# Kernel optimization log

Hardware: AMD Instinct MI355X
Metric: run time of the kernel (lower is better)

The kernel has to match this reference:

```python
import jax, jax.numpy as jnp
import numpy as np

N, E = 20000, 320000
C, IN_NF, HID_NF, OUT_NF, CH_NF, RAD_NF = 14, 128, 128, 128, 16, 128
CONSTANT = 1.0
LN_EPS = 1e-5
SCALE = 0.02


def _pool_matrix(c, dtype):
    # RollerPooling buffer: pool_matrix[i] averages a sliding window of size c-i
    ones = np.ones((c, c), dtype=np.float32)
    mats = [(np.triu(ones) - np.triu(ones, k=c - i)) / float(c - i) for i in range(c)]
    return jnp.asarray(np.stack(mats), dtype=dtype)


def setup_inputs() -> dict:
    key = jax.random.key(0)
    ks = jax.random.split(key, 32)
    h = jax.random.normal(ks[0], (N, IN_NF), jnp.float32)
    x = jax.random.normal(ks[1], (N, C, 3), jnp.float32)
    row = jax.random.randint(ks[2], (E,), 0, N)
    off = jax.random.randint(ks[3], (E,), 1, N)
    col = (row + off) % N  # guarantees row != col (avoids zero-distance edges)
    channel_attr = jax.random.normal(ks[4], (N, C, CH_NF), jnp.float32)
    w = jax.random.uniform(ks[5], (N, C), jnp.float32, 0.1, 1.0)
    keep = jax.random.uniform(ks[6], (N, C)) > 0.3
    keep = keep.at[:, 0].set(True)  # every node has >=1 active channel
    channel_weights = w * keep.astype(jnp.float32)

    def lin(k, o, i):
        k1, k2 = jax.random.split(k)
        return (jax.random.normal(k1, (o, i), jnp.float32) * SCALE,
                jax.random.normal(k2, (o,), jnp.float32) * SCALE)

    radial_W, radial_b = lin(ks[7], RAD_NF, CH_NF * CH_NF)
    e1_W, e1_b = lin(ks[8], HID_NF, 2 * IN_NF + RAD_NF)
    e2_W, e2_b = lin(ks[9], HID_NF, HID_NF)
    att_W, att_b = lin(ks[10], 1, HID_NF)
    c1_W, c1_b = lin(ks[11], HID_NF, HID_NF)
    c2_W, c2_b = lin(ks[12], C, HID_NF)
    n1_W, n1_b = lin(ks[13], HID_NF, IN_NF + HID_NF)
    n2_W, n2_b = lin(ks[14], OUT_NF, HID_NF)
    ln_g = jnp.ones((OUT_NF,), jnp.float32)
    ln_b = jnp.zeros((OUT_NF,), jnp.float32)
    return dict(h=h, x=x, row=row, col=col, channel_attr=channel_attr,
                channel_weights=channel_weights,
                radial_W=radial_W, radial_b=radial_b,
                e1_W=e1_W, e1_b=e1_b, e2_W=e2_W, e2_b=e2_b,
                att_W=att_W, att_b=att_b,
                c1_W=c1_W, c1_b=c1_b, c2_W=c2_W, c2_b=c2_b,
                n1_W=n1_W, n1_b=n1_b, n2_W=n2_W, n2_b=n2_b,
                ln_g=ln_g, ln_b=ln_b)


def _scatter_mean(v, idx, n):
    s = jnp.zeros((n,) + v.shape[1:], v.dtype).at[idx].add(v)
    cnt = jnp.zeros((n,), v.dtype).at[idx].add(1.0)
    cnt = jnp.maximum(cnt, 1.0)
    return s / cnt.reshape((n,) + (1,) * (v.ndim - 1))


def _forward(h, x, row, col, channel_attr, channel_weights,
             radial_W, radial_b, e1_W, e1_b, e2_W, e2_b, att_W, att_b,
             c1_W, c1_b, c2_W, c2_b, n1_W, n1_b, n2_W, n2_b, ln_g, ln_b):
    n, c, d = x.shape
    silu = jax.nn.silu
    coord_r = x[row]           # [E, C, 3]
    coord_c = x[col]
    # pairwise channel distances [E, C, C]
    dist = jnp.linalg.norm(coord_r[:, :, None, :] - coord_c[:, None, :, :], axis=-1)
    cw_r = channel_weights[row]
    cw_c = channel_weights[col]
    coord_msg = dist * (cw_r[:, :, None] * cw_c[:, None, :])
    # attr_r^T @ coord_msg @ attr_c -> [E, CH_NF, CH_NF]
    radial = jnp.einsum('eca,ecd,edb->eab', channel_attr[row], coord_msg, channel_attr[col])
    radial = radial.reshape(radial.shape[0], -1)
    rnorm = jnp.linalg.norm(radial, axis=-1, keepdims=True) + CONSTANT
    radial = (radial @ radial_W.T + radial_b) / rnorm  # [E, RAD_NF]
    # pooled column coord over active channels
    mask = (channel_weights != 0).astype(x.dtype)      # [N, C]
    csum = mask.sum(-1)                                # [N]
    pooled_col = (coord_c * mask[col][:, :, None]).sum(1) / csum[col][:, None]  # [E, 3]
    coord_diff = coord_r - pooled_col[:, None, :]      # [E, C, 3]
    # edge MLP (dropout = identity in eval)
    ef = jnp.concatenate([h[row], h[col], radial], axis=-1)
    ef = silu(ef @ e1_W.T + e1_b)
    ef = silu(ef @ e2_W.T + e2_b)
    ef = ef * jax.nn.sigmoid(ef @ att_W.T + att_b)     # att_mlp (hidden_nf == input_nf)
    # coord MLP + roller pooling
    ch = silu(ef @ c1_W.T + c1_b) @ c2_W.T + c2_b      # [E, C]
    tsize = csum[row].astype(jnp.int32) - 1            # [E] in [0, C-1]
    pool_mat = _pool_matrix(c, x.dtype)                # [C, C, C]
    pooled = jnp.einsum('eij,ej->ei', pool_mat[tsize], ch)  # [E, C]
    trans = coord_diff * pooled[:, :, None]            # [E, C, 3]
    x_out = x + _scatter_mean(trans, row, n)
    agg = _scatter_mean(ef, col, n)
    nh = jnp.concatenate([h, agg], axis=-1)
    nh = silu(nh @ n1_W.T + n1_b) @ n2_W.T + n2_b
    y = h + nh
    mu = y.mean(-1, keepdims=True)
    var = ((y - mu) ** 2).mean(-1, keepdims=True)
    h_out = (y - mu) / jnp.sqrt(var + LN_EPS) * ln_g + ln_b
    return h_out, x_out


def reference(h, x, row, col, channel_attr, channel_weights,
              radial_W, radial_b, e1_W, e1_b, e2_W, e2_b, att_W, att_b,
              c1_W, c1_b, c2_W, c2_b, n1_W, n1_b, n2_W, n2_b, ln_g, ln_b):
    return _forward(h, x, row, col, channel_attr, channel_weights,
                    radial_W, radial_b, e1_W, e1_b, e2_W, e2_b, att_W, att_b,
                    c1_W, c1_b, c2_W, c2_b, n1_W, n1_b, n2_W, n2_b, ln_g, ln_b)
```

## Files before the change

### kernel.cpp

```cpp
#include <hip/hip_runtime.h>
#include <math.h>

#define NN 20000
#define NE 320000

typedef const float* fp;
typedef short short8 __attribute__((ext_vector_type(8)));
typedef short short4v __attribute__((ext_vector_type(4)));
typedef float f32x4 __attribute__((ext_vector_type(4)));

__device__ __forceinline__ short F2B(float f) {
    unsigned u = __float_as_uint(f);
    return (short)((u + 0x7fffu + ((u >> 16) & 1u)) >> 16);
}
__device__ __forceinline__ short F2Bf(float f) {
    return (short)((__float_as_uint(f) + 0x8000u) >> 16);
}
__device__ __forceinline__ float B2F(short s) {
    return __uint_as_float(((unsigned)(unsigned short)s) << 16);
}
__device__ __forceinline__ float siluf(float v) { return v / (1.f + __expf(-v)); }

#if defined(__has_builtin)
#if __has_builtin(__builtin_amdgcn_mfma_f32_16x16x16bf16_1k)
#define MFMA16_BUILTIN 1
__device__ __forceinline__ f32x4 mfma16(short4v a, short4v b, f32x4 c) {
    return __builtin_amdgcn_mfma_f32_16x16x16bf16_1k(a, b, c, 0, 0, 0);
}
#elif __has_builtin(__builtin_amdgcn_mfma_f32_16x16x16_bf16)
#define MFMA16_BUILTIN 1
__device__ __forceinline__ f32x4 mfma16(short4v a, short4v b, f32x4 c) {
    return __builtin_amdgcn_mfma_f32_16x16x16_bf16(a, b, c, 0, 0, 0);
}
#endif
#endif
#ifndef MFMA16_BUILTIN
__device__ __forceinline__ f32x4 mfma16(short4v a, short4v b, f32x4 c) {
    f32x4 d;
    asm volatile("s_nop 1\n\tv_mfma_f32_16x16x16_bf16 %0, %1, %2, %3\n\ts_nop 7\n\ts_nop 7"
                 : "=v"(d) : "v"(a), "v"(b), "v"(c));
    return d;
}
#endif

__global__ void k_prep_w(fp e1W, fp e2W, fp c1W, fp c2W, fp n1W, fp n2W,
                         short* __restrict__ wb) {
    int i = blockIdx.x * 256 + threadIdx.x;
    if (i >= 149504) return;
    if (i >= 32768 && i < 65536) return;
    float v;
    if (i < 32768)       { int o = i >> 8, k = i & 255; v = e1W[o * 384 + k]; }
    else if (i < 81920)  v = e2W[i - 65536];
    else if (i < 98304)  v = c1W[i - 81920];
    else if (i < 100352) { int q = i - 98304; v = (q < 1792) ? c2W[q] : 0.f; }
    else if (i < 133120) v = n1W[i - 100352];
    else                 v = n2W[i - 133120];
    wb[i] = F2B(v);
}

__global__ void k_fold(fp e1W, fp rW, fp rB, short* __restrict__ wb,
                       float* __restrict__ bc) {
    int o = blockIdx.x, k = threadIdx.x;
    float acc = 0.f;
    for (int m = 0; m < 128; m++) acc += e1W[o * 384 + 256 + m] * rW[m * 256 + k];
    wb[32768 + o * 256 + k] = F2B(acc);
    if (k == 0) {
        float b = 0.f;
        for (int m = 0; m < 128; m++) b += e1W[o * 384 + 256 + m] * rB[m];
        bc[o] = b;
    }
}

__global__ void k_prep_h(fp h, short* __restrict__ hb) {
    int i = blockIdx.x * 256 + threadIdx.x;
    if (i < NN * 128) hb[i] = F2B(h[i]);
}

__global__ void k_prep_attrT(fp attr, fp cw, short* __restrict__ aT) {
    int i = blockIdx.x * 256 + threadIdx.x;
    if (i >= NN * 256) return;
    int n = i >> 8, rem = i & 255, c = rem >> 4, a = rem & 15;
    float v = (c < 14) ? attr[(size_t)n * 224 + c * 16 + a] * cw[n * 14 + c] : 0.f;
    aT[(size_t)n * 256 + a * 16 + c] = F2B(v);
}

__global__ void k_node_pre(fp x, fp cw, float* __restrict__ csum, float* __restrict__ pool) {
    int n = blockIdx.x * blockDim.x + threadIdx.x;
    if (n >= NN) return;
    float cnt = 0.f, px = 0.f, py = 0.f, pz = 0.f;
#pragma unroll
    for (int c = 0; c < 14; c++) {
        float w = cw[n * 14 + c];
        if (w != 0.f) {
            cnt += 1.f;
            px += x[(n * 14 + c) * 3 + 0];
            py += x[(n * 14 + c) * 3 + 1];
            pz += x[(n * 14 + c) * 3 + 2];
        }
    }
    if (cnt < 1.f) cnt = 1.f;
    csum[n] = cnt;
    pool[n * 3 + 0] = px / cnt;
    pool[n * 3 + 1] = py / cnt;
    pool[n * 3 + 2] = pz / cnt;
}

__global__ void k_count(const int* __restrict__ row, const int* __restrict__ col,
                        int* __restrict__ cnt_r, int* __restrict__ cnt_c) {
    int e = blockIdx.x * 256 + threadIdx.x;
    if (e >= NE) return;
    atomicAdd(&cnt_c[col[e]], 1);
    atomicAdd(&cnt_r[row[e]], 1);
}

__global__ void k_scan(int* __restrict__ cnt0, int* __restrict__ cnt1,
                       int* __restrict__ off0, int* __restrict__ off1) {
    __shared__ int part[256];
    const int tid = threadIdx.x;
    for (int a = 0; a < 2; a++) {
        int* cnt = a ? cnt1 : cnt0;
        int* off = a ? off1 : off0;
        int c0 = tid * 79, c1 = c0 + 79;
        if (c1 > 20000) c1 = 20000;
        int s = 0;
        for (int i = c0; i < c1; i++) s += cnt[i];
        part[tid] = s;
        __syncthreads();
        if (tid == 0) {
            int r = 0;
            for (int i = 0; i < 256; i++) { int t = part[i]; part[i] = r; r += t; }
        }
        __syncthreads();
        int run = part[tid];
        for (int i = c0; i < c1; i++) {
            int cv = cnt[i];
            off[i] = run;
            cnt[i] = run;
            run += cv;
        }
        if (tid == 255) off[20000] = run;
        __syncthreads();
    }
}

__global__ void k_fill(const int* __restrict__ row, const int* __restrict__ col,
                       int* __restrict__ head_r, int* __restrict__ head_c,
                       int* __restrict__ eidx_r,
                       int* __restrict__ row_s, int* __restrict__ col_s) {
    int e = blockIdx.x * 256 + threadIdx.x;
    if (e >= NE) return;
    int r = row[e], c = col[e];
    int pc = atomicAdd(&head_c[c], 1);
    row_s[pc] = r;
    col_s[pc] = c;
    int pr = atomicAdd(&head_r[r], 1);
    eidx_r[pr] = pc;
}

__device__ __forceinline__ void gemm_lds(const short* __restrict__ A, int sA,
                                         const short* __restrict__ W, int Ws, int K,
                                         int mt, int nt0, int nts, f32x4* acc) {
    const int lane = threadIdx.x & 63;
    const short* ap = A + (mt * 16 + (lane & 15)) * sA + ((lane >> 4) * 8);
    for (int k0 = 0; k0 < K; k0 += 32) {
        short8 a = *(const short8*)(ap + k0);
#pragma unroll
        for (int t = 0; t < nts; t++) {
            short8 b = *(const short8*)(W + ((nt0 + t) * 16 + (lane & 15)) * Ws + k0 + ((lane >> 4) * 8));
            acc[t] = __builtin_amdgcn_mfma_f32_16x16x32_bf16(a, b, acc[t], 0, 0, 0);
        }
    }
}
__device__ __forceinline__ void gemm_grow(const short* __restrict__ arow,
                                          const short* __restrict__ W, int Ws, int K,
                                          int nt0, int nts, f32x4* acc) {
    const int lane = threadIdx.x & 63;
    for (int k0 = 0; k0 < K; k0 += 32) {
        short8 a = *(const short8*)(arow + k0);
#pragma unroll
        for (int t = 0; t < nts; t++) {
            short8 b = *(const short8*)(W + ((nt0 + t) * 16 + (lane & 15)) * Ws + k0 + ((lane >> 4) * 8));
            acc[t] = __builtin_amdgcn_mfma_f32_16x16x32_bf16(a, b, acc[t], 0, 0, 0);
        }
    }
}

__global__ __launch_bounds__(256, 2) void k_hw(const short* __restrict__ hb,
                                               const short* __restrict__ wb,
                                               short* __restrict__ H12) {
    __shared__ __attribute__((aligned(16))) short A[32 * 136];
    const int tid = threadIdx.x, lane = tid & 63, w = tid >> 6;
    const int bb = lane & 15, quad = lane >> 4;
    const int mt = w & 1, nh = w >> 1, nb0 = blockIdx.x * 32;
    for (int p = tid; p < 512; p += 256) {
        int i = p >> 4, v = p & 15;
        *(short8*)(A + i * 136 + v * 8) = *(const short8*)(hb + (size_t)(nb0 + i) * 128 + v * 8);
    }
    __syncthreads();
    f32x4 acc[4];
#pragma unroll
    for (int t = 0; t < 4; t++) acc[t] = (f32x4){0.f, 0.f, 0.f, 0.f};
    gemm_lds(A, 136, wb, 256, 128, mt, nh * 4, 4, acc);
#pragma unroll
    for (int t = 0; t < 4; t++)
#pragma unroll
        for (int i = 0; i < 4; i++) {
            int m = mt * 16 + quad * 4 + i, n = (nh * 4 + t) * 16 + bb;
            H12[(size_t)(nb0 + m) * 256 + n] = F2Bf(acc[t][i]);
        }
#pragma unroll
    for (int t = 0; t < 4; t++) acc[t] = (f32x4){0.f, 0.f, 0.f, 0.f};
    gemm_lds(A, 136, wb + 128, 256, 128, mt, nh * 4, 4, acc);
#pragma unroll
    for (int t = 0; t < 4; t++)
#pragma unroll
        for (int i = 0; i < 4; i++) {
            int m = mt * 16 + quad * 4 + i, n = (nh * 4 + t) * 16 + bb;
            H12[(size_t)(nb0 + m) * 256 + 128 + n] = F2Bf(acc[t][i]);
        }
}

__global__ __launch_bounds__(256, 6) void k_radial(
    fp x, const int* __restrict__ row_s, const int* __restrict__ col_s,
    const short* __restrict__ attrT,
    const short* __restrict__ wb, const float* __restrict__ bc,
    short* __restrict__ e1p) {
    __shared__ __attribute__((aligned(16))) short Ar[32 * 264];
    __shared__ float xc2[4][2][48];
    __shared__ float s_inv[32];
    const int tid = threadIdx.x, lane = tid & 63, w = tid >> 6;
    const int bb = lane & 15, quad = lane >> 4;
    const int e0 = blockIdx.x * 32;
    const short* Wc = wb + 32768;

#pragma unroll 2
    for (int m = 0; m < 8; m++) {
        const int ep = e0 + w * 8 + m;
        const int r = row_s[ep], c = col_s[ep];
        const int bufi = m & 1;
        short4v arv = *(const short4v*)(attrT + (size_t)r * 256 + bb * 16 + quad * 4);
        short4v acv = *(const short4v*)(attrT + (size_t)c * 256 + bb * 16 + quad * 4);
        if (lane < 42) xc2[w][bufi][lane] = x[(size_t)c * 42 + lane];
        const int iic = bb < 14 ? bb : 13;
        float xr0 = x[(size_t)r * 42 + iic * 3];
        float xr1 = x[(size_t)r * 42 + iic * 3 + 1];
        float xr2 = x[(size_t)r * 42 + iic * 3 + 2];
        short4v msgv;
#pragma unroll
        for (int t = 0; t < 4; t++) {
            int jj = quad * 4 + t, jc = jj < 14 ? jj : 13;
            float dx = xr0 - xc2[w][bufi][jc * 3];
            float dy = xr1 - xc2[w][bufi][jc * 3 + 1];
            float dz = xr2 - xc2[w][bufi][jc * 3 + 2];
            msgv[t] = F2Bf(sqrtf(dx * dx + dy * dy + dz * dz));
        }
        f32x4 t2 = mfma16(msgv, acv, (f32x4){0.f, 0.f, 0.f, 0.f});
        short4v t2v;
#pragma unroll
        for (int g = 0; g < 4; g++) t2v[g] = F2Bf(t2[g]);
        f32x4 rad = mfma16(arv, t2v, (f32x4){0.f, 0.f, 0.f, 0.f});
        float ss = rad[0] * rad[0] + rad[1] * rad[1] + rad[2] * rad[2] + rad[3] * rad[3];
#pragma unroll
        for (int off = 32; off > 0; off >>= 1) ss += __shfl_xor(ss, off, 64);
        float inv = 1.f / (sqrtf(ss) + 1.f);
        if (lane == 0) s_inv[w * 8 + m] = inv;
#pragma unroll
        for (int g = 0; g < 4; g++)
            Ar[(w * 8 + m) * 264 + (quad * 4 + g) * 16 + bb] = F2Bf(rad[g] * inv);
    }
    __syncthreads();

    f32x4 acc[2][2];
#pragma unroll
    for (int mt = 0; mt < 2; mt++)
#pragma unroll
        for (int nt = 0; nt < 2; nt++) acc[mt][nt] = (f32x4){0.f, 0.f, 0.f, 0.f};
    for (int k0 = 0; k0 < 256; k0 += 32) {
        short8 a0 = *(const short8*)(Ar + bb * 264 + k0 + quad * 8);
        short8 a1 = *(const short8*)(Ar + (16 + bb) * 264 + k0 + quad * 8);
        short8 b0 = *(const short8*)(Wc + (size_t)(w * 32 + bb) * 256 + k0 + quad * 8);
        short8 b1 = *(const short8*)(Wc + (size_t)(w * 32 + 16 + bb) * 256 + k0 + quad * 8);
        acc[0][0] = __builtin_amdgcn_mfma_f32_16x16x32_bf16(a0, b0, acc[0][0], 0, 0, 0);
        acc[0][1] = __builtin_amdgcn_mfma_f32_16x16x32_bf16(a0, b1, acc[0][1], 0, 0, 0);
        acc[1][0] = __builtin_amdgcn_mfma_f32_16x16x32_bf16(a1, b0, acc[1][0], 0, 0, 0);
        acc[1][1] = __builtin_amdgcn_mfma_f32_16x16x32_bf16(a1, b1, acc[1][1], 0, 0, 0);
    }
    __syncthreads();

    short* E1 = Ar;
#pragma unroll
    for (int mt = 0; mt < 2; mt++)
#pragma unroll
        for (int nt = 0; nt < 2; nt++)
#pragma unroll
            for (int i = 0; i < 4; i++) {
                int m = mt * 16 + quad * 4 + i, n = w * 32 + nt * 16 + bb;
                E1[m * 136 + n] = F2Bf(acc[mt][nt][i] + s_inv[m] * bc[n]);
            }
    __syncthreads();
    for (int p = tid; p < 512; p += 256) {
        int e = p >> 4, v = p & 15;
        *(short8*)(e1p + (size_t)(e0 + e) * 128 + v * 8) = *(const short8*)(E1 + e * 136 + v * 8);
    }
}

__global__ __launch_bounds__(256, 8) void k_edge_split(
    const int* __restrict__ row_s, const int* __restrict__ col_s,
    const short* __restrict__ H12, short* __restrict__ e1p,
    const short* __restrict__ wb,
    fp e1B, fp e2B, fp aW, fp aB, fp c1B, fp c2B,
    const float* __restrict__ csum, const float* __restrict__ poolc,
    short* __restrict__ pooledb, float* __restrict__ pcrec) {
    __shared__ __attribute__((aligned(16))) short V1[32 * 136];
    __shared__ __attribute__((aligned(16))) short V2[32 * 136];
    __shared__ int s_r[32], s_c[32];
    __shared__ float s_ch[32][14];
    __shared__ float s_red8[32][8], s_gate[32];

    const int tid = threadIdx.x, lane = tid & 63, w = tid >> 6;
    const int bb = lane & 15, quad = lane >> 4;
    const int mt = w & 1, nh = w >> 1;
    const int e0 = blockIdx.x * 32;

    if (tid < 32) { s_r[tid] = row_s[e0 + tid]; s_c[tid] = col_s[e0 + tid]; }
    __syncthreads();

    for (int p = tid; p < 512; p += 256) {
        int e = p >> 4, v = p & 15;
        short8 hr = *(const short8*)(H12 + (size_t)s_r[e] * 256 + v * 8);
        short8 hc = *(const short8*)(H12 + (size_t)s_c[e] * 256 + 128 + v * 8);
        short8 pp = *(const short8*)(e1p + (size_t)(e0 + e) * 128 + v * 8);
        short8 o;
#pragma unroll
        for (int j = 0; j < 8; j++)
            o[j] = F2Bf(siluf(B2F(hr[j]) + B2F(hc[j]) + B2F(pp[j]) + e1B[v * 8 + j]));
        *(short8*)(V1 + e * 136 + v * 8) = o;
    }
    __syncthreads();

    f32x4 acc[4];
#pragma unroll
    for (int t = 0; t < 4; t++) acc[t] = (f32x4){0.f, 0.f, 0.f, 0.f};
    gemm_lds(V1, 136, wb + 65536, 128, 128, mt, nh * 4, 4, acc);
#pragma unroll
    for (int t = 0; t < 4; t++)
#pragma unroll
        for (int i = 0; i < 4; i++) {
            int m = mt * 16 + quad * 4 + i, n = (nh * 4 + t) * 16 + bb;
            V2[m * 136 + n] = F2Bf(siluf(acc[t][i] + e2B[n]));
        }
    __syncthreads();

    {
        int e = tid >> 3, j = tid & 7;
        float s = 0.f;
        for (int f = j * 16; f < j * 16 + 16; f++) s += B2F(V2[e * 136 + f]) * aW[f];
        s_red8[e][j] = s;
    }
    __syncthreads();
    if (tid < 32) {
        float s = 0.f;
#pragma unroll
        for (int j = 0; j < 8; j++) s += s_red8[tid][j];
        s_gate[tid] = 1.f / (1.f + __expf(-(s + aB[0])));
    }
    __syncthreads();
    for (int p = tid; p < 512; p += 256) {
        int e = p >> 4, v = p & 15;
        short8 a = *(const short8*)(V2 + e * 136 + v * 8);
        short8 o;
#pragma unroll
        for (int j = 0; j < 8; j++) o[j] = F2Bf(B2F(a[j]) * s_gate[e]);
        *(short8*)(V1 + e * 136 + v * 8) = o;
        *(short8*)(e1p + (size_t)(e0 + e) * 128 + v * 8) = o;
    }
    __syncthreads();

#pragma unroll
    for (int t = 0; t < 4; t++) acc[t] = (f32x4){0.f, 0.f, 0.f, 0.f};
    gemm_lds(V1, 136, wb + 81920, 128, 128, mt, nh * 4, 4, acc);
    __syncthreads();
#pragma unroll
    for (int t = 0; t < 4; t++)
#pragma unroll
        for (int i = 0; i < 4; i++) {
            int m = mt * 16 + quad * 4 + i, n = (nh * 4 + t) * 16 + bb;
            V2[m * 136 + n] = F2Bf(siluf(acc[t][i] + c1B[n]));
        }
    __syncthreads();

    if (nh == 0) {
        f32x4 a4 = (f32x4){0.f, 0.f, 0.f, 0.f};
        gemm_lds(V2, 136, wb + 98304, 128, 128, mt, 0, 1, &a4);
#pragma unroll
        for (int i = 0; i < 4; i++) {
            int m = mt * 16 + quad * 4 + i;
            if (bb < 14) s_ch[m][bb] = a4[i] + c2B[bb];
        }
    }
    __syncthreads();

    if (tid < 32) {
        int t = (int)(csum[s_r[tid]] + 0.5f) - 1;
        if (t < 0) t = 0; if (t > 13) t = 13;
        int Wd = 14 - t;
        for (int i = 0; i < 14; i++) {
            int jend = i + Wd - 1; if (jend > 13) jend = 13;
            float a = 0.f;
            for (int j = i; j <= jend; j++) a += s_ch[tid][j];
            pooledb[(size_t)(e0 + tid) * 16 + i] = F2Bf(a / (float)Wd);
        }
        int c = s_c[tid];
        float4 pc = make_float4(poolc[c * 3 + 0], poolc[c * 3 + 1], poolc[c * 3 + 2], 0.f);
        *(float4*)(pcrec + (size_t)(e0 + tid) * 4) = pc;
    }
}

__global__ __launch_bounds__(256, 3) void k_edge_fused(
    fp x, const int* __restrict__ row, const int* __restrict__ col,
    fp attr, fp cw, const short* __restrict__ hb, const short* __restrict__ wb,
    fp e1B, fp e2B, fp aW, fp aB, fp c1B, fp c2B,
    const float* __restrict__ bc, const float* __restrict__ csum,
    const float* __restrict__ poolc,
    float* __restrict__ xacc, float* __restrict__ agg,
    float* __restrict__ cntr, float* __restrict__ cntc) {
    __shared__ __attribute__((aligned(16))) short R1[13056];
    __shared__ float s_xr2[32 * 42];
    __shared__ float T[4][352];
    __shared__ int   s_r[32], s_c[32];
    __shared__ float s_inv[32];
    __shared__ float s_ch[32][14], s_pool[32][14];
    __shared__ float s_red8[32][8];
    __shared__ float s_gate[32];

    const int tid = threadIdx.x, lane = tid & 63, w = tid >> 6;
    const int bb = lane & 15, quad = lane >> 4;

    if (tid < 32) { s_r[tid] = row[blockIdx.x * 32 + tid]; s_c[tid] = col[blockIdx.x * 32 + tid]; }
    __syncthreads();

    float* slot = T[w];
    float* t2w = slot + 72;
    for (int i8 = 0; i8 < 8; i8++) {
        const int e = w * 8 + i8;
        const int r = s_r[e], cl = s_c[e];
        if (lane < 42) {
            s_xr2[e * 42 + lane] = x[(size_t)r * 42 + lane];
            slot[lane] = x[(size_t)cl * 42 + lane];
        }
        if (lane < 14)      slot[42 + lane] = cw[r * 14 + lane];
        else if (lane < 28) slot[56 + (lane - 14)] = cw[cl * 14 + (lane - 14)];
        __builtin_amdgcn_wave_barrier();

        const int iic = bb < 14 ? bb : 13;
        float xr0 = s_xr2[e * 42 + iic * 3], xr1 = s_xr2[e * 42 + iic * 3 + 1],
              xr2v = s_xr2[e * 42 + iic * 3 + 2];
        float cwri = slot[42 + iic];
        short8 msgv, acv;
#pragma unroll
        for (int t = 0; t < 8; t++) {
            int jj = quad * 8 + t, jc = jj < 14 ? jj : 13;
            float dx = xr0 - slot[jc * 3], dy = xr1 - slot[jc * 3 + 1], dz = xr2v - slot[jc * 3 + 2];
            float m = sqrtf(dx * dx + dy * dy + dz * dz) * cwri * slot[56 + jc];
            msgv[t] = (bb < 14 && jj < 14) ? F2B(m) : (short)0;
            acv[t] = F2B(attr[(size_t)cl * 224 + jc * 16 + bb]);
        }
        f32x4 t2 = (f32x4){0.f, 0.f, 0.f, 0.f};
        t2 = __builtin_amdgcn_mfma_f32_16x16x32_bf16(msgv, acv, t2, 0, 0, 0);
#pragma unroll
        for (int g = 0; g < 4; g++) t2w[(quad * 4 + g) * 17 + bb] = t2[g];
        __builtin_amdgcn_wave_barrier();

        short8 arv, t2v;
#pragma unroll
        for (int t = 0; t < 8; t++) {
            int kk = quad * 8 + t, kc = kk < 16 ? kk : 15;
            t2v[t] = F2B(t2w[kc * 17 + bb]);
            arv[t] = (kk < 14) ? F2B(attr[(size_t)r * 224 + kk * 16 + bb]) : (short)0;
        }
        f32x4 rad = (f32x4){0.f, 0.f, 0.f, 0.f};
        rad = __builtin_amdgcn_mfma_f32_16x16x32_bf16(arv, t2v, rad, 0, 0, 0);

        float ss = rad[0] * rad[0] + rad[1] * rad[1] + rad[2] * rad[2] + rad[3] * rad[3];
#pragma unroll
        for (int off = 32; off > 0; off >>= 1) ss += __shfl_xor(ss, off, 64);
        float inv = 1.f / (sqrtf(ss) + 1.f);
        if (lane == 0) s_inv[e] = inv;
#pragma unroll
        for (int g = 0; g < 4; g++)
            R1[e * 264 + (quad * 4 + g) * 16 + bb] = F2B(rad[g] * inv);
        __builtin_amdgcn_wave_barrier();
    }
    __syncthreads();

    const int mt = w & 1, nh = w >> 1;
    const int m_ = mt * 16 + bb;
    f32x4 acc[4];
#pragma unroll
    for (int t = 0; t < 4; t++) acc[t] = (f32x4){0.f, 0.f, 0.f, 0.f};
    {
        const short* ar_ = hb + (size_t)s_r[m_] * 128 + quad * 8;
        const short* ac_ = hb + (size_t)s_c[m_] * 128 + quad * 8;
        gemm_grow(ar_, wb, 256, 128, nh * 4, 4, acc);
        gemm_grow(ac_, wb + 128, 256, 128, nh * 4, 4, acc);
        gemm_lds(R1, 264, wb + 32768, 256, 256, mt, nh * 4, 4, acc);
    }
    __syncthreads();
    short* V1 = R1;
    short* V2 = R1 + 4352;
    short* C1O = R1 + 8704;
#pragma unroll
    for (int t = 0; t < 4; t++)
#pragma unroll
        for (int i = 0; i < 4; i++) {
            int m = mt * 16 + quad * 4 + i, n = (nh * 4 + t) * 16 + bb;
            V1[m * 136 + n] = F2B(siluf(acc[t][i] + e1B[n] + bc[n] * s_inv[m]));
        }
    __syncthreads();

#pragma unroll
    for (int t = 0; t < 4; t++) acc[t] = (f32x4){0.f, 0.f, 0.f, 0.f};
    gemm_lds(V1, 136, wb + 65536, 128, 128, mt, nh * 4, 4, acc);
    __syncthreads();
#pragma unroll
    for (int t = 0; t < 4; t++)
#pragma unroll
        for (int i = 0; i < 4; i++) {
            int m = mt * 16 + quad * 4 + i, n = (nh * 4 + t) * 16 + bb;
            V2[m * 136 + n] = F2B(siluf(acc[t][i] + e2B[n]));
        }
    __syncthreads();

    {
        int e = tid >> 3, j = tid & 7;
        float s = 0.f;
        for (int f = j * 16; f < j * 16 + 16; f++) s += B2F(V2[e * 136 + f]) * aW[f];
        s_red8[e][j] = s;
    }
    __syncthreads();
    if (tid < 32) {
        float s = 0.f;
#pragma unroll
        for (int j = 0; j < 8; j++) s += s_red8[tid][j];
        s_gate[tid] = 1.f / (1.f + __expf(-(s + aB[0])));
    }
    __syncthreads();
    for (int p = tid; p < 32 * 128; p += 256) {
        int e = p >> 7, f = p & 127;
        V1[e * 136 + f] = F2B(B2F(V2[e * 136 + f]) * s_gate[e]);
    }
    __syncthreads();

#pragma unroll
    for (int t = 0; t < 4; t++) acc[t] = (f32x4){0.f, 0.f, 0.f, 0.f};
    gemm_lds(V1, 136, wb + 81920, 128, 128, mt, nh * 4, 4, acc);
    __syncthreads();
#pragma unroll
    for (int t = 0; t < 4; t++)
#pragma unroll
        for (int i = 0; i < 4; i++) {
            int m = mt * 16 + quad * 4 + i, n = (nh * 4 + t) * 16 + bb;
            C1O[m * 136 + n] = F2B(siluf(acc[t][i] + c1B[n]));
        }
    __syncthreads();

    if (nh == 0) {
        f32x4 a4 = (f32x4){0.f, 0.f, 0.f, 0.f};
        gemm_lds(C1O, 136, wb + 98304, 128, 128, mt, 0, 1, &a4);
#pragma unroll
        for (int i = 0; i < 4; i++) {
            int m = mt * 16 + quad * 4 + i;
            if (bb < 14) s_ch[m][bb] = a4[i] + c2B[bb];
        }
    }
    __syncthreads();

    if (tid < 32) {
        int t = (int)(csum[s_r[tid]] + 0.5f) - 1;
        if (t < 0) t = 0; if (t > 13) t = 13;
        int Wd = 14 - t;
        for (int i = 0; i < 14; i++) {
            int jend = i + Wd - 1; if (jend > 13) jend = 13;
            float a = 0.f;
            for (int j = i; j <= jend; j++) a += s_ch[tid][j];
            s_pool[tid][i] = a / (float)Wd;
        }
    }
    __syncthreads();

    for (int p = tid; p < 32 * 42; p += 256) {
        int e = p / 42, q = p - e * 42, i = q / 3, d = q - i * 3;
        float diff = s_xr2[e * 42 + q] - poolc[s_c[e] * 3 + d];
        atomicAdd(&xacc[(size_t)s_r[e] * 42 + q], diff * s_pool[e][i]);
    }
    for (int p = tid; p < 32 * 128; p += 256) {
        int e = p >> 7, f = p & 127;
        atomicAdd(&agg[(size_t)s_c[e] * 128 + f], B2F(V1[e * 136 + f]));
    }
    if (tid < 32) {
        atomicAdd(&cntr[s_r[tid]], 1.f);
        atomicAdd(&cntc[s_c[tid]], 1.f);
    }
}

__global__ __launch_bounds__(256, 4) void k_node_post_csr(
    fp h, fp x, const short* __restrict__ wb,
    fp n1B, fp n2B, fp lng, fp lnb,
    const short* __restrict__ efb, const short* __restrict__ pooledb,
    const int* __restrict__ off_c, const int* __restrict__ off_r,
    const int* __restrict__ eidx_r, const float* __restrict__ pcrec,
    float* __restrict__ outh, float* __restrict__ outx) {
    __shared__ __attribute__((aligned(16))) short nA[32 * 264];
    __shared__ __attribute__((aligned(16))) short nMid[32 * 136];
    __shared__ float nred8[32][8];
    __shared__ float nmu[32], nrs[32];
    float* nY = (float*)nA;

    const int tid = threadIdx.x;
    const int wave = tid >> 6, mt = wave & 1, nh = wave >> 1;
    const int lane = tid & 63, bb = lane & 15, quad = lane >> 4;
    const int nb0 = blockIdx.x * 32;
    const short* n1Wb = wb + 100352;
    const short* n2Wb = wb + 133120;

    for (int p = tid; p < 32 * 128; p += 256) {
        int i = p >> 7, f = p & 127;
        nA[i * 264 + f] = F2Bf(h[(size_t)(nb0 + i) * 128 + f]);
    }
    {
        const int ni = tid >> 3, seg = tid & 7;
        const int n = nb0 + ni;
        const int beg = off_c[n], end = off_c[n + 1];
        float av[16];
#pragma unroll
        for (int j = 0; j < 16; j++) av[j] = 0.f;
        for (int k = beg; k < end; k++) {
            short8 u0 = *(const short8*)(efb + (size_t)k * 128 + seg * 16);
            short8 u1 = *(const short8*)(efb + (size_t)k * 128 + seg * 16 + 8);
#pragma unroll
            for (int j = 0; j < 8; j++) { av[j] += B2F(u0[j]); av[8 + j] += B2F(u1[j]); }
        }
        float inv = 1.f / fmaxf((float)(end - beg), 1.f);
#pragma unroll
        for (int j = 0; j < 16; j++)
            nA[ni * 264 + 128 + seg * 16 + j] = F2Bf(av[j] * inv);
    }
    __syncthreads();

    f32x4 acc[4];
#pragma unroll
    for (int t = 0; t < 4; t++) acc[t] = (f32x4){0.f, 0.f, 0.f, 0.f};
    gemm_lds(nA, 264, n1Wb, 256, 256, mt, nh * 4, 4, acc);
#pragma unroll
    for (int t = 0; t < 4; t++)
#pragma unroll
        for (int i = 0; i < 4; i++) {
            int m = mt * 16 + quad * 4 + i, n = (nh * 4 + t) * 16 + bb;
            nMid[m * 136 + n] = F2Bf(siluf(acc[t][i] + n1B[n]));
        }
    __syncthreads();

#pragma unroll
    for (int t = 0; t < 4; t++) acc[t] = (f32x4){0.f, 0.f, 0.f, 0.f};
    gemm_lds(nMid, 136, n2Wb, 128, 128, mt, nh * 4, 4, acc);
#pragma unroll
    for (int t = 0; t < 4; t++)
#pragma unroll
        for (int i = 0; i < 4; i++) {
            int m = mt * 16 + quad * 4 + i, n = (nh * 4 + t) * 16 + bb;
            nY[m * 128 + n] = acc[t][i] + n2B[n] + h[(size_t)(nb0 + m) * 128 + n];
        }
    __syncthreads();

    {
        int i = tid >> 3, j = tid & 7;
        float s = 0.f;
        for (int f = j * 16; f < j * 16 + 16; f++) s += nY[i * 128 + f];
        nred8[i][j] = s;
    }
    __syncthreads();
    if (tid < 32) {
        float s = 0.f;
#pragma unroll
        for (int j = 0; j < 8; j++) s += nred8[tid][j];
        nmu[tid] = s * (1.f / 128.f);
    }
    __syncthreads();
    {
        int i = tid >> 3, j = tid & 7;
        float mu = nmu[i], s = 0.f;
        for (int f = j * 16; f < j * 16 + 16; f++) { float d = nY[i * 128 + f] - mu; s += d * d; }
        nred8[i][j] = s;
    }
    __syncthreads();
    if (tid < 32) {
        float s = 0.f;
#pragma unroll
        for (int j = 0; j < 8; j++) s += nred8[tid][j];
        nrs[tid] = rsqrtf(s * (1.f / 128.f) + 1e-5f);
    }
    __syncthreads();
    for (int p = tid; p < 32 * 128; p += 256) {
        int i = p >> 7, f = p & 127;
        outh[(size_t)(nb0 + i) * 128 + f] = (nY[i * 128 + f] - nmu[i]) * nrs[i] * lng[f] + lnb[f];
    }
    for (int p = tid; p < 32 * 3; p += 256) {
        int i = p / 3, d = p - i * 3;
        int n = nb0 + i;
        int beg = off_r[n], end = off_r[n + 1];
        float Q[14], P[14];
#pragma unroll
        for (int ic = 0; ic < 14; ic++) { Q[ic] = 0.f; P[ic] = 0.f; }
        for (int k = beg; k < end; k++) {
            int sp = eidx_r[k];
            short8 p0 = *(const short8*)(pooledb + (size_t)sp * 16);
            short8 p1 = *(const short8*)(pooledb + (size_t)sp * 16 + 8);
            float4 pc = *(const float4*)(pcrec + (size_t)sp * 4);
            float pcd = (d == 0) ? pc.x : ((d == 1) ? pc.y : pc.z);
#pragma unroll
            for (int ic = 0; ic < 8; ic++) { float pw = B2F(p0[ic]); P[ic] += pw; Q[ic] += pw * pcd; }
#pragma unroll
            for (int ic = 0; ic < 6; ic++) { float pw = B2F(p1[ic]); P[8 + ic] += pw; Q[8 + ic] += pw * pcd; }
        }
        float invd = 1.f / fmaxf((float)(end - beg), 1.f);
#pragma unroll
        for (int ic = 0; ic < 14; ic++) {
            float x0 = x[(size_t)n * 42 + ic * 3 + d];
            outx[(size_t)n * 42 + ic * 3 + d] = x0 + (x0 * P[ic] - Q[ic]) * invd;
        }
    }
}

__global__ __launch_bounds__(256, 2) void k_node_post(
    fp h, fp x, const short* __restrict__ wb,
    fp n1B, fp n2B, fp lng, fp lnb,
    const float* __restrict__ agg, const float* __restrict__ cntc,
    const float* __restrict__ xacc, const float* __restrict__ cntr,
    float* __restrict__ outh, float* __restrict__ outx) {
    __shared__ __attribute__((aligned(16))) short nA[32 * 264];
    __shared__ __attribute__((aligned(16))) short nMid[32 * 136];
    __shared__ float nY[32][128];
    __shared__ float nred8[32][8];
    __shared__ float nmu[32], nrs[32];

    const int tid = threadIdx.x;
    const int wave = tid >> 6, mt = wave & 1, nh = wave >> 1;
    const int lane = tid & 63, bb = lane & 15, quad = lane >> 4;
    const int nb0 = blockIdx.x * 32;
    const short* n1Wb = wb + 100352;
    const short* n2Wb = wb + 133120;

    for (int p = tid; p < 32 * 128; p += 256) {
        int i = p >> 7, f = p & 127;
        int n = nb0 + i;
        nA[i * 264 + f] = F2Bf(h[(size_t)n * 128 + f]);
        float cc = cntc[n]; if (cc < 1.f) cc = 1.f;
        nA[i * 264 + 128 + f] = F2Bf(agg[(size_t)n * 128 + f] / cc);
    }
    __syncthreads();

    f32x4 acc[4];
#pragma unroll
    for (int t = 0; t < 4; t++) acc[t] = (f32x4){0.f, 0.f, 0.f, 0.f};
    gemm_lds(nA, 264, n1Wb, 256, 256, mt, nh * 4, 4, acc);
#pragma unroll
    for (int t = 0; t < 4; t++)
#pragma unroll
        for (int i = 0; i < 4; i++) {
            int m = mt * 16 + quad * 4 + i, n = (nh * 4 + t) * 16 + bb;
            nMid[m * 136 + n] = F2Bf(siluf(acc[t][i] + n1B[n]));
        }
    __syncthreads();

#pragma unroll
    for (int t = 0; t < 4; t++) acc[t] = (f32x4){0.f, 0.f, 0.f, 0.f};
    gemm_lds(nMid, 136, n2Wb, 128, 128, mt, nh * 4, 4, acc);
#pragma unroll
    for (int t = 0; t < 4; t++)
#pragma unroll
        for (int i = 0; i < 4; i++) {
            int m = mt * 16 + quad * 4 + i, n = (nh * 4 + t) * 16 + bb;
            nY[m][n] = acc[t][i] + n2B[n] + h[(size_t)(nb0 + m) * 128 + n];
        }
    __syncthreads();

    {
        int i = tid >> 3, j = tid & 7;
        float s = 0.f;
        for (int f = j * 16; f < j * 16 + 16; f++) s += nY[i][f];
        nred8[i][j] = s;
    }
    __syncthreads();
    if (tid < 32) {
        float s = 0.f;
#pragma unroll
        for (int j = 0; j < 8; j++) s += nred8[tid][j];
        nmu[tid] = s * (1.f / 128.f);
    }
    __syncthreads();
    {
        int i = tid >> 3, j = tid & 7;
        float mu = nmu[i], s = 0.f;
        for (int f = j * 16; f < j * 16 + 16; f++) { float d = nY[i][f] - mu; s += d * d; }
        nred8[i][j] = s;
    }
    __syncthreads();
    if (tid < 32) {
        float s = 0.f;
#pragma unroll
        for (int j = 0; j < 8; j++) s += nred8[tid][j];
        nrs[tid] = rsqrtf(s * (1.f / 128.f) + 1e-5f);
    }
    __syncthreads();
    for (int p = tid; p < 32 * 128; p += 256) {
        int i = p >> 7, f = p & 127;
        outh[(size_t)(nb0 + i) * 128 + f] = (nY[i][f] - nmu[i]) * nrs[i] * lng[f] + lnb[f];
    }
    for (int p = tid; p < 32 * 42; p += 256) {
        int i = p / 42, q = p - i * 42;
        int n = nb0 + i;
        float cr = cntr[n]; if (cr < 1.f) cr = 1.f;
        outx[(size_t)n * 42 + q] = x[(size_t)n * 42 + q] + xacc[(size_t)n * 42 + q] / cr;
    }
}

extern "C" void kernel_launch(void* const* d_in, const int* in_sizes, int n_in,
                              void* d_out, int out_size, void* d_ws, size_t ws_size,
                              hipStream_t stream) {
    fp h   = (fp)d_in[0];
    fp x   = (fp)d_in[1];
    const int* row = (const int*)d_in[2];
    const int* col = (const int*)d_in[3];
    fp attr= (fp)d_in[4];
    fp cw  = (fp)d_in[5];
    fp rW  = (fp)d_in[6];  fp rB  = (fp)d_in[7];
    fp e1W = (fp)d_in[8];  fp e1B = (fp)d_in[9];
    fp e2W = (fp)d_in[10]; fp e2B = (fp)d_in[11];
    fp aW  = (fp)d_in[12]; fp aB  = (fp)d_in[13];
    fp c1W = (fp)d_in[14]; fp c1B = (fp)d_in[15];
    fp c2W = (fp)d_in[16]; fp c2B = (fp)d_in[17];
    fp n1W = (fp)d_in[18]; fp n1B = (fp)d_in[19];
    fp n2W = (fp)d_in[20]; fp n2B = (fp)d_in[21];
    fp lng = (fp)d_in[22]; fp lnb = (fp)d_in[23];

    float* ws    = (float*)d_ws;
    int*   wsi   = (int*)d_ws;
    float* xacc  = ws;
    float* agg   = ws + 840000;
    float* cntr  = ws + 3400000;
    float* cntc  = ws + 3420000;
    float* csum  = ws + 3440000;
    float* pool  = ws + 3460000;
    float* bc    = ws + 3520000;
    short* hb    = (short*)(ws + 3520128);
    short* wb    = (short*)(ws + 4800128);
    short* H12   = (short*)(ws + 4874880);
    short* e1p   = (short*)(ws + 7434880);
    short* attrT = (short*)(ws + 27914880);
    short* pooledb = attrT;
    float* pcrec   = ws + 3520128;

    int* off_c  = wsi + 0;
    int* off_r  = wsi + 20002;
    int* head_c = wsi + 40004;
    int* head_r = wsi + 60004;
    int* eidx_r = wsi + 80004;
    int* row_s  = wsi + 400004;
    int* col_s  = wsi + 720004;

    const size_t need = 30474880ull * 4ull;

    if (ws_size >= need) {
        hipMemsetAsync(head_c, 0, 40000 * sizeof(int), stream);
        k_count<<<(NE + 255) / 256, 256, 0, stream>>>(row, col, head_r, head_c);
        k_scan<<<1, 256, 0, stream>>>(head_c, head_r, off_c, off_r);
        k_fill<<<(NE + 255) / 256, 256, 0, stream>>>(row, col, head_r, head_c,
                                                     eidx_r, row_s, col_s);

        k_prep_w<<<(149504 + 255) / 256, 256, 0, stream>>>(e1W, e2W, c1W, c2W, n1W, n2W, wb);
        k_fold<<<128, 256, 0, stream>>>(e1W, rW, rB, wb, bc);
        k_prep_h<<<(NN * 128 + 255) / 256, 256, 0, stream>>>(h, hb);
        k_node_pre<<<(NN + 255) / 256, 256, 0, stream>>>(x, cw, csum, pool);
        k_prep_attrT<<<(NN * 256 + 255) / 256, 256, 0, stream>>>(attr, cw, attrT);
        k_hw<<<NN / 32, 256, 0, stream>>>(hb, wb, H12);
        k_radial<<<NE / 32, 256, 0, stream>>>(x, row_s, col_s, attrT, wb, bc, e1p);
        k_edge_split<<<NE / 32, 256, 0, stream>>>(row_s, col_s, H12, e1p, wb,
                                                  e1B, e2B, aW, aB, c1B, c2B,
                                                  csum, pool, pooledb, pcrec);
        float* outh = (float*)d_out;
        float* outx = outh + NN * 128;
        k_node_post_csr<<<NN / 32, 256, 0, stream>>>(h, x, wb, n1B, n2B, lng, lnb,
                                                     e1p, pooledb,
                                                     off_c, off_r, eidx_r,
                                                     pcrec, outh, outx);
    } else {
        hipMemsetAsync(d_ws, 0, 3440000 * sizeof(float), stream);
        k_prep_w<<<(149504 + 255) / 256, 256, 0, stream>>>(e1W, e2W, c1W, c2W, n1W, n2W, wb);
        k_fold<<<128, 256, 0, stream>>>(e1W, rW, rB, wb, bc);
        k_prep_h<<<(NN * 128 + 255) / 256, 256, 0, stream>>>(h, hb);
        k_node_pre<<<(NN + 255) / 256, 256, 0, stream>>>(x, cw, csum, pool);
        k_edge_fused<<<NE / 32, 256, 0, stream>>>(x, row, col, attr, cw, hb, wb,
                                                  e1B, e2B, aW, aB, c1B, c2B,
                                                  bc, csum, pool, xacc, agg, cntr, cntc);
        float* outh = (float*)d_out;
        float* outx = outh + NN * 128;
        k_node_post<<<NN / 32, 256, 0, stream>>>(h, x, wb, n1B, n2B, lng, lnb,
                                                 agg, cntc, xacc, cntr, outh, outx);
    }
}
```

Baseline: 708.5 us.

## Fuse radial and edge-MLP kernels, keep radial output in LDS

Merges k_radial and k_edge_split into one k_edge kernel. The folded radial/e1 projection now stays in shared memory instead of being written to and re-read from global memory, and row/col indices are loaded once per block. The pooled buffer is packed to 14 bf16 per edge instead of 16 and moved to its own workspace region, which shrinks the gather traffic in the node-post kernel. The fused kernel uses more registers and shared memory, and launch bounds change from 6 and 8 to 7, which may cut occupancy.

```diff
diff --git a/kernel.cpp b/kernel.cpp
--- a/kernel.cpp
+++ b/kernel.cpp
@@ -220,23 +220,37 @@
         }
 }
 
-__global__ __launch_bounds__(256, 6) void k_radial(
+__global__ __launch_bounds__(256, 7) void k_edge(
     fp x, const int* __restrict__ row_s, const int* __restrict__ col_s,
-    const short* __restrict__ attrT,
+    const short* __restrict__ attrT, const short* __restrict__ H12,
     const short* __restrict__ wb, const float* __restrict__ bc,
-    short* __restrict__ e1p) {
-    __shared__ __attribute__((aligned(16))) short Ar[32 * 264];
+    fp e1B, fp e2B, fp aW, fp aB, fp c1B, fp c2B,
+    const float* __restrict__ csum, const float* __restrict__ poolc,
+    short* __restrict__ e1p, short* __restrict__ pooledb,
+    float* __restrict__ pcrec) {
+    __shared__ __attribute__((aligned(16))) short U[8704];
     __shared__ float xc2[4][2][48];
     __shared__ float s_inv[32];
+    __shared__ int s_r[32], s_c[32];
+    __shared__ float s_ch[32][14];
+    __shared__ float s_red8[32][8], s_gate[32];
+
     const int tid = threadIdx.x, lane = tid & 63, w = tid >> 6;
     const int bb = lane & 15, quad = lane >> 4;
+    const int mt = w & 1, nh = w >> 1;
     const int e0 = blockIdx.x * 32;
     const short* Wc = wb + 32768;
+    short* Ar = U;
+    short* V1 = U;
+    short* V2 = U + 4352;
+
+    if (tid < 32) { s_r[tid] = row_s[e0 + tid]; s_c[tid] = col_s[e0 + tid]; }
+    __syncthreads();
 
 #pragma unroll 2
     for (int m = 0; m < 8; m++) {
-        const int ep = e0 + w * 8 + m;
-        const int r = row_s[ep], c = col_s[ep];
+        const int ei = w * 8 + m;
+        const int r = s_r[ei], c = s_c[ei];
         const int bufi = m & 1;
         short4v arv = *(const short4v*)(attrT + (size_t)r * 256 + bb * 16 + quad * 4);
         short4v acv = *(const short4v*)(attrT + (size_t)c * 256 + bb * 16 + quad * 4);
@@ -263,73 +277,46 @@
 #pragma unroll
         for (int off = 32; off > 0; off >>= 1) ss += __shfl_xor(ss, off, 64);
         float inv = 1.f / (sqrtf(ss) + 1.f);
-        if (lane == 0) s_inv[w * 8 + m] = inv;
+        if (lane == 0) s_inv[ei] = inv;
 #pragma unroll
         for (int g = 0; g < 4; g++)
-            Ar[(w * 8 + m) * 264 + (quad * 4 + g) * 16 + bb] = F2Bf(rad[g] * inv);
-    }
-    __syncthreads();
-
-    f32x4 acc[2][2];
-#pragma unroll
-    for (int mt = 0; mt < 2; mt++)
-#pragma unroll
-        for (int nt = 0; nt < 2; nt++) acc[mt][nt] = (f32x4){0.f, 0.f, 0.f, 0.f};
+            Ar[ei * 264 + (quad * 4 + g) * 16 + bb] = F2Bf(rad[g] * inv);
+    }
+    __syncthreads();
+
+    f32x4 racc[2][2];
+#pragma unroll
+    for (int a = 0; a < 2; a++)
+#pragma unroll
+        for (int b = 0; b < 2; b++) racc[a][b] = (f32x4){0.f, 0.f, 0.f, 0.f};
     for (int k0 = 0; k0 < 256; k0 += 32) {
         short8 a0 = *(const short8*)(Ar + bb * 264 + k0 + quad * 8);
         short8 a1 = *(const short8*)(Ar + (16 + bb) * 264 + k0 + quad * 8);
         short8 b0 = *(const short8*)(Wc + (size_t)(w * 32 + bb) * 256 + k0 + quad * 8);
         short8 b1 = *(const short8*)(Wc + (size_t)(w * 32 + 16 + bb) * 256 + k0 + quad * 8);
-        acc[0][0] = __builtin_amdgcn_mfma_f32_16x16x32_bf16(a0, b0, acc[0][0], 0, 0, 0);
-        acc[0][1] = __builtin_amdgcn_mfma_f32_16x16x32_bf16(a0, b1, acc[0][1], 0, 0, 0);
-        acc[1][0] = __builtin_amdgcn_mfma_f32_16x16x32_bf16(a1, b0, acc[1][0], 0, 0, 0);
-        acc[1][1] = __builtin_amdgcn_mfma_f32_16x16x32_bf16(a1, b1, acc[1][1], 0, 0, 0);
-    }
-    __syncthreads();
-
-    short* E1 = Ar;
-#pragma unroll
-    for (int mt = 0; mt < 2; mt++)
-#pragma unroll
-        for (int nt = 0; nt < 2; nt++)
+        racc[0][0] = __builtin_amdgcn_mfma_f32_16x16x32_bf16(a0, b0, racc[0][0], 0, 0, 0);
+        racc[0][1] = __builtin_amdgcn_mfma_f32_16x16x32_bf16(a0, b1, racc[0][1], 0, 0, 0);
+        racc[1][0] = __builtin_amdgcn_mfma_f32_16x16x32_bf16(a1, b0, racc[1][0], 0, 0, 0);
+        racc[1][1] = __builtin_amdgcn_mfma_f32_16x16x32_bf16(a1, b1, racc[1][1], 0, 0, 0);
+    }
+    __syncthreads();
+
+#pragma unroll
+    for (int a = 0; a < 2; a++)
+#pragma unroll
+        for (int b = 0; b < 2; b++)
 #pragma unroll
             for (int i = 0; i < 4; i++) {
-                int m = mt * 16 + quad * 4 + i, n = w * 32 + nt * 16 + bb;
-                E1[m * 136 + n] = F2Bf(acc[mt][nt][i] + s_inv[m] * bc[n]);
+                int m = a * 16 + quad * 4 + i, n = w * 32 + b * 16 + bb;
+                V1[m * 136 + n] = F2Bf(racc[a][b][i] + s_inv[m] * bc[n]);
             }
-    __syncthreads();
-    for (int p = tid; p < 512; p += 256) {
-        int e = p >> 4, v = p & 15;
-        *(short8*)(e1p + (size_t)(e0 + e) * 128 + v * 8) = *(const short8*)(E1 + e * 136 + v * 8);
-    }
-}
-
-__global__ __launch_bounds__(256, 8) void k_edge_split(
-    const int* __restrict__ row_s, const int* __restrict__ col_s,
-    const short* __restrict__ H12, short* __restrict__ e1p,
-    const short* __restrict__ wb,
-    fp e1B, fp e2B, fp aW, fp aB, fp c1B, fp c2B,
-    const float* __restrict__ csum, const float* __restrict__ poolc,
-    short* __restrict__ pooledb, float* __restrict__ pcrec) {
-    __shared__ __attribute__((aligned(16))) short V1[32 * 136];
-    __shared__ __attribute__((aligned(16))) short V2[32 * 136];
-    __shared__ int s_r[32], s_c[32];
-    __shared__ float s_ch[32][14];
-    __shared__ float s_red8[32][8], s_gate[32];
-
-    const int tid = threadIdx.x, lane = tid & 63, w = tid >> 6;
-    const int bb = lane & 15, quad = lane >> 4;
-    const int mt = w & 1, nh = w >> 1;
-    const int e0 = blockIdx.x * 32;
-
-    if (tid < 32) { s_r[tid] = row_s[e0 + tid]; s_c[tid] = col_s[e0 + tid]; }
     __syncthreads();
 
     for (int p = tid; p < 512; p += 256) {
         int e = p >> 4, v = p & 15;
         short8 hr = *(const short8*)(H12 + (size_t)s_r[e] * 256 + v * 8);
         short8 hc = *(const short8*)(H12 + (size_t)s_c[e] * 256 + 128 + v * 8);
-        short8 pp = *(const short8*)(e1p + (size_t)(e0 + e) * 128 + v * 8);
+        short8 pp = *(const short8*)(V1 + e * 136 + v * 8);
         short8 o;
 #pragma unroll
         for (int j = 0; j < 8; j++)
@@ -408,7 +395,7 @@
             int jend = i + Wd - 1; if (jend > 13) jend = 13;
             float a = 0.f;
             for (int j = i; j <= jend; j++) a += s_ch[tid][j];
-            pooledb[(size_t)(e0 + tid) * 16 + i] = F2Bf(a / (float)Wd);
+            pooledb[(size_t)(e0 + tid) * 14 + i] = F2Bf(a / (float)Wd);
         }
         int c = s_c[tid];
         float4 pc = make_float4(poolc[c * 3 + 0], poolc[c * 3 + 1], poolc[c * 3 + 2], 0.f);
@@ -713,14 +700,17 @@
         for (int ic = 0; ic < 14; ic++) { Q[ic] = 0.f; P[ic] = 0.f; }
         for (int k = beg; k < end; k++) {
             int sp = eidx_r[k];
-            short8 p0 = *(const short8*)(pooledb + (size_t)sp * 16);
-            short8 p1 = *(const short8*)(pooledb + (size_t)sp * 16 + 8);
+            const int* pp = (const int*)(pooledb + (size_t)sp * 14);
             float4 pc = *(const float4*)(pcrec + (size_t)sp * 4);
             float pcd = (d == 0) ? pc.x : ((d == 1) ? pc.y : pc.z);
 #pragma unroll
-            for (int ic = 0; ic < 8; ic++) { float pw = B2F(p0[ic]); P[ic] += pw; Q[ic] += pw * pcd; }
-#pragma unroll
-            for (int ic = 0; ic < 6; ic++) { float pw = B2F(p1[ic]); P[8 + ic] += pw; Q[8 + ic] += pw * pcd; }
+            for (int u2 = 0; u2 < 7; u2++) {
+                int u = pp[u2];
+                float pw0 = B2F((short)(u & 0xffff));
+                float pw1 = B2F((short)(((unsigned)u) >> 16));
+                P[2 * u2] += pw0;     Q[2 * u2] += pw0 * pcd;
+                P[2 * u2 + 1] += pw1; Q[2 * u2 + 1] += pw1 * pcd;
+            }
         }
         float invd = 1.f / fmaxf((float)(end - beg), 1.f);
 #pragma unroll
@@ -857,7 +847,7 @@
     short* H12   = (short*)(ws + 4874880);
     short* e1p   = (short*)(ws + 7434880);
     short* attrT = (short*)(ws + 27914880);
-    short* pooledb = attrT;
+    short* pooledb = (short*)(ws + 1040004);
     float* pcrec   = ws + 3520128;
 
     int* off_c  = wsi + 0;
@@ -883,10 +873,9 @@
         k_node_pre<<<(NN + 255) / 256, 256, 0, stream>>>(x, cw, csum, pool);
         k_prep_attrT<<<(NN * 256 + 255) / 256, 256, 0, stream>>>(attr, cw, attrT);
         k_hw<<<NN / 32, 256, 0, stream>>>(hb, wb, H12);
-        k_radial<<<NE / 32, 256, 0, stream>>>(x, row_s, col_s, attrT, wb, bc, e1p);
-        k_edge_split<<<NE / 32, 256, 0, stream>>>(row_s, col_s, H12, e1p, wb,
-                                                  e1B, e2B, aW, aB, c1B, c2B,
-                                                  csum, pool, pooledb, pcrec);
+        k_edge<<<NE / 32, 256, 0, stream>>>(x, row_s, col_s, attrT, H12, wb, bc,
+                                            e1B, e2B, aW, aB, c1B, c2B,
+                                            csum, pool, e1p, pooledb, pcrec);
         float* outh = (float*)d_out;
         float* outx = outh + NN * 128;
         k_node_post_csr<<<NN / 32, 256, 0, stream>>>(h, x, wb, n1B, n2B, lng, lnb,
```

Result: no change. 704.1 us (-0.6%).
